# Performance work log

Hardware: AMD Instinct MI355X
Metric: run time of the kernel (lower is better)

The kernel has to match this reference:

```python
import jax, jax.numpy as jnp
import numpy as np

NUM_NODES = 50000
NUM_EDGES = 600000
IN_DIM = 128
HID = 128
OUT_DIM = 10
NUM_GRAPHS = 64


def setup_inputs() -> dict:
    key = jax.random.key(0)
    ks = jax.random.split(key, 12)
    x = jax.random.normal(ks[0], (NUM_NODES, IN_DIM), dtype=jnp.float32)
    edge_index = jax.random.randint(ks[1], (2, NUM_EDGES), 0, NUM_NODES, dtype=jnp.int64)
    batch = jnp.sort(jax.random.randint(ks[2], (NUM_NODES,), 0, NUM_GRAPHS, dtype=jnp.int64))
    s = 0.05
    W1 = jax.random.normal(ks[3], (IN_DIM, HID), dtype=jnp.float32) * s
    b1 = jnp.zeros((HID,), dtype=jnp.float32)
    W2 = jax.random.normal(ks[4], (HID, HID), dtype=jnp.float32) * s
    b2 = jnp.zeros((HID,), dtype=jnp.float32)
    W3 = jax.random.normal(ks[5], (HID, HID), dtype=jnp.float32) * s
    b3 = jnp.zeros((HID,), dtype=jnp.float32)
    Wlin = jax.random.normal(ks[6], (HID, OUT_DIM), dtype=jnp.float32) * s
    blin = jnp.zeros((OUT_DIM,), dtype=jnp.float32)
    return {"x": x, "edge_index": edge_index, "batch": batch,
            "W1": W1, "b1": b1, "W2": W2, "b2": b2, "W3": W3, "b3": b3,
            "Wlin": Wlin, "blin": blin}


def _gcn_conv(x, W, b, src, dst, norm):
    # h = X W ; out[i] = sum_{(j->i)} norm_e * h[j] ; + bias
    h = x @ W                                   # [N, H]
    msg = h[src] * norm[:, None]                # [E+N, H] gather + scale
    out = jax.ops.segment_sum(msg, dst, num_segments=x.shape[0])  # scatter-add
    return out + b


def reference(x, edge_index, batch, W1, b1, W2, b2, W3, b3, Wlin, blin):
    N = x.shape[0]
    # add self loops (PyG GCNConv default)
    loops = jnp.arange(N, dtype=edge_index.dtype)
    src = jnp.concatenate([edge_index[0], loops])
    dst = jnp.concatenate([edge_index[1], loops])
    # symmetric normalization D^{-1/2} (A+I) D^{-1/2}; degree on target nodes
    deg = jax.ops.segment_sum(jnp.ones_like(dst, dtype=x.dtype), dst, num_segments=N)
    dinv = jnp.where(deg > 0, jax.lax.rsqrt(deg), 0.0)
    norm = dinv[src] * dinv[dst]

    h = jax.nn.relu(_gcn_conv(x, W1, b1, src, dst, norm))   # dropout = identity (eval)
    h = jax.nn.relu(_gcn_conv(h, W2, b2, src, dst, norm))
    h = jax.nn.relu(_gcn_conv(h, W3, b3, src, dst, norm))

    # global mean pool over graphs
    sums = jax.ops.segment_sum(h, batch, num_segments=NUM_GRAPHS)          # [G, H]
    cnts = jax.ops.segment_sum(jnp.ones((N,), dtype=h.dtype), batch, num_segments=NUM_GRAPHS)
    pooled = sums / jnp.maximum(cnts, 1.0)[:, None]
    return pooled @ Wlin + blin                                            # [G, OUT]
```

## Files before the change

### kernel.cpp

```cpp
#include <hip/hip_runtime.h>
#include <hip/hip_bf16.h>
#include <hip/hip_fp16.h>


#define HID 128
#define NGRAPH 64

typedef _Float16 half8v __attribute__((ext_vector_type(8)));
typedef float floatx4 __attribute__((ext_vector_type(4)));

__device__ __forceinline__ int idx_at(const void* p, long long i, int f64) {
    if (f64) return (int)((const long long*)p)[i];
    return ((const int*)p)[i];
}

__global__ void init_kernel(const int* __restrict__ ei, int* __restrict__ flag,
                            int* __restrict__ counts, float* __restrict__ pooled,
                            uint4* __restrict__ csr4, int N, int nCsr4) {
    int i = blockIdx.x * blockDim.x + threadIdx.x;
    int stride = gridDim.x * blockDim.x;
    if (i < N) counts[i] = 0;
    if (i < NGRAPH * HID) pooled[i] = 0.f;
    unsigned fillv = (unsigned)N | ((unsigned)N << 16);
    uint4 fv = make_uint4(fillv, fillv, fillv, fillv);
    for (int j = i; j < nCsr4; j += stride) csr4[j] = fv;
    if (blockIdx.x == 0) {
        __shared__ int cnt;
        if (threadIdx.x == 0) cnt = 0;
        __syncthreads();
        int z = 0;
        for (int k = threadIdx.x; k < 2048; k += 256)
            if (ei[2 * k + 1] == 0) z++;
        atomicAdd(&cnt, z);
        __syncthreads();
        if (threadIdx.x == 0) *flag = (cnt > 1024) ? 1 : 0;
    }
}

__global__ void hist_kernel(const void* __restrict__ ei, const int* __restrict__ flag,
                            int* __restrict__ counts, int E, int N) {
    int e = blockIdx.x * blockDim.x + threadIdx.x;
    if (e >= E) return;
    int f64 = *flag;
    int d = idx_at(ei, (long long)E + e, f64);
    if ((unsigned)d < (unsigned)N) atomicAdd(&counts[d], 1);
}

__device__ __forceinline__ int wave_incl_scan(int v, int lane) {
#pragma unroll
    for (int off = 1; off < 64; off <<= 1) {
        int u = __shfl_up(v, off);
        if (lane >= off) v += u;
    }
    return v;
}

__global__ __launch_bounds__(256) void blocksum_kernel(const int* __restrict__ counts,
                                                       int* __restrict__ bsums, int N) {
    int i = blockIdx.x * 256 + threadIdx.x;
    int v = (i < N) ? ((counts[i] + 7) & ~7) : 0;
    int lane = threadIdx.x & 63, w = threadIdx.x >> 6;
#pragma unroll
    for (int off = 32; off > 0; off >>= 1) v += __shfl_down(v, off);
    __shared__ int ws[4];
    if (lane == 0) ws[w] = v;
    __syncthreads();
    if (threadIdx.x == 0) bsums[blockIdx.x] = ws[0] + ws[1] + ws[2] + ws[3];
}

__global__ __launch_bounds__(256) void scanb_kernel(int* __restrict__ bsums, int nb) {
    int t = threadIdx.x;
    int lane = t & 63, w = t >> 6;
    int v = (t < nb) ? bsums[t] : 0;
    int iv = wave_incl_scan(v, lane);
    __shared__ int wsum[4];
    if (lane == 63) wsum[w] = iv;
    __syncthreads();
    int add = 0;
    for (int k = 0; k < w; ++k) add += wsum[k];
    if (t < nb) bsums[t] = iv - v + add;
}

__global__ __launch_bounds__(256) void fill_kernel(const int* __restrict__ counts,
                                                   const int* __restrict__ bsums,
                                                   int* __restrict__ rowstart,
                                                   int* __restrict__ cursor,
                                                   float* __restrict__ dinv, int N) {
    int i = blockIdx.x * 256 + threadIdx.x;
    int c = (i < N) ? counts[i] : 0;
    int cp = (c + 7) & ~7;
    int lane = threadIdx.x & 63, w = threadIdx.x >> 6;
    int iv = wave_incl_scan(cp, lane);
    __shared__ int wsum[4];
    if (lane == 63) wsum[w] = iv;
    __syncthreads();
    int add = bsums[blockIdx.x];
    for (int k = 0; k < w; ++k) add += wsum[k];
    int excl = iv - cp + add;
    if (i < N) {
        rowstart[i] = excl;
        cursor[i] = excl;
        dinv[i] = rsqrtf((float)(c + 1));
        if (i == N - 1) rowstart[N] = excl + cp;
    }
}

__global__ void scatter_kernel(const void* __restrict__ ei, const int* __restrict__ flag,
                               int* __restrict__ cursor,
                               unsigned short* __restrict__ csr_src, int E, int N) {
    int e = blockIdx.x * blockDim.x + threadIdx.x;
    if (e >= E) return;
    int f64 = *flag;
    int s = idx_at(ei, e, f64);
    int d = idx_at(ei, (long long)E + e, f64);
    if ((unsigned)s >= (unsigned)N || (unsigned)d >= (unsigned)N) return;
    int pos = atomicAdd(&cursor[d], 1);
    csr_src[pos] = (unsigned short)s;
}

__global__ __launch_bounds__(256) void prep_kernel(const float* __restrict__ x,
                                                   const float* __restrict__ dinv,
                                                   __half2* __restrict__ xs,
                                                   __half2* __restrict__ hsA,
                                                   __half2* __restrict__ hsB,
                                                   const float* __restrict__ W1,
                                                   const float* __restrict__ W2,
                                                   const float* __restrict__ W3,
                                                   half8v* __restrict__ wf,
                                                   int N, int n2) {
    if (blockIdx.x < 24) {
        int which = blockIdx.x >> 3;
        const float* W = which == 0 ? W1 : (which == 1 ? W2 : W3);
        int t = (blockIdx.x & 7) * 256 + threadIdx.x;
        int lane = t & 63;
        int nt = (t >> 6) & 7;
        int kblk = t >> 9;
        int n = nt * 16 + (lane & 15);
        int kbase = kblk * 32 + (lane >> 4) * 8;
        half8v v;
#pragma unroll
        for (int j = 0; j < 8; ++j) v[j] = (_Float16)W[(size_t)(kbase + j) * 128 + n];
        wf[which * 2048 + t] = v;
    } else if (blockIdx.x == 24) {
        int t = threadIdx.x;
        __half2 z = __floats2half2_rn(0.f, 0.f);
        if (t < 64) xs[(size_t)N * 64 + t] = z;
        else if (t < 128) hsA[(size_t)N * 64 + (t - 64)] = z;
        else if (t < 192) hsB[(size_t)N * 64 + (t - 128)] = z;
    } else {
        int i = (blockIdx.x - 25) * 256 + threadIdx.x;
        if (i >= n2) return;
        float dv = dinv[i >> 6];
        float2 v = ((const float2*)x)[i];
        xs[i] = __floats2half2_rn(dv * v.x, dv * v.y);
    }
}

__global__ __launch_bounds__(256) void agg_kernel(const __half2* __restrict__ xs,
                                                  const int* __restrict__ rowstart,
                                                  const unsigned short* __restrict__ csr_src,
                                                  const float* __restrict__ dinv,
                                                  __half2* __restrict__ out, int N) {
    int wid = (blockIdx.x * blockDim.x + threadIdx.x) >> 6;
    int lane = threadIdx.x & 63;
    if (wid >= N) return;
    float di = dinv[wid];
    float2 s0 = __half22float2(xs[(size_t)wid * 64 + lane]);
    float accx = s0.x, accy = s0.y;
    float bccx = 0.f, bccy = 0.f;
    int e0 = rowstart[wid], e1 = rowstart[wid + 1];
    for (int e = e0; e < e1; e += 8) {
        uint4 q = *(const uint4*)(csr_src + e);
        int s0i = q.x & 0xffff, s1i = q.x >> 16;
        int s2i = q.y & 0xffff, s3i = q.y >> 16;
        int s4i = q.z & 0xffff, s5i = q.z >> 16;
        int s6i = q.w & 0xffff, s7i = q.w >> 16;
        __half2 v0 = xs[(size_t)s0i * 64 + lane];
        __half2 v1 = xs[(size_t)s1i * 64 + lane];
        __half2 v2 = xs[(size_t)s2i * 64 + lane];
        __half2 v3 = xs[(size_t)s3i * 64 + lane];
        __half2 v4 = xs[(size_t)s4i * 64 + lane];
        __half2 v5 = xs[(size_t)s5i * 64 + lane];
        __half2 v6 = xs[(size_t)s6i * 64 + lane];
        __half2 v7 = xs[(size_t)s7i * 64 + lane];
        float2 f0 = __half22float2(v0), f1 = __half22float2(v1);
        float2 f2 = __half22float2(v2), f3 = __half22float2(v3);
        float2 f4 = __half22float2(v4), f5 = __half22float2(v5);
        float2 f6 = __half22float2(v6), f7 = __half22float2(v7);
        accx += f0.x + f2.x; accy += f0.y + f2.y;
        bccx += f1.x + f3.x; bccy += f1.y + f3.y;
        accx += f4.x + f6.x; accy += f4.y + f6.y;
        bccx += f5.x + f7.x; bccy += f5.y + f7.y;
    }
    out[(size_t)wid * 64 + lane] = __floats2half2_rn(di * (accx + bccx),
                                                     di * (accy + bccy));
}

template <bool SCALED>
__global__ __launch_bounds__(256) void gemm_mfma(const __half2* __restrict__ A16,
                                                 const half8v* __restrict__ wf,
                                                 const float* __restrict__ bias,
                                                 const float* __restrict__ dinv,
                                                 __half2* __restrict__ O16, int M) {
    int wid = threadIdx.x >> 6, lane = threadIdx.x & 63;
    int rowTile = blockIdx.x * 64 + wid * 16;
    int hi = lane >> 4;
    int arow = rowTile + (lane & 15);
    if (arow >= M) arow = M - 1;
    const half8v* Arow = (const half8v*)((const _Float16*)A16 + (size_t)arow * 128);

    floatx4 acc[8];
#pragma unroll
    for (int nt = 0; nt < 8; ++nt) acc[nt] = (floatx4){0.f, 0.f, 0.f, 0.f};

#pragma unroll
    for (int kb = 0; kb < 4; ++kb) {
        half8v a = Arow[kb * 4 + hi];
#pragma unroll
        for (int nt = 0; nt < 8; ++nt) {
            half8v w = wf[(kb * 8 + nt) * 64 + lane];
            acc[nt] = __builtin_amdgcn_mfma_f32_16x16x32_f16(a, w, acc[nt], 0, 0, 0);
        }
    }

    int ocol_lo = lane & 15;
    int orow0 = rowTile + hi * 4;
    float dv[4];
#pragma unroll
    for (int r = 0; r < 4; ++r) {
        int orow = orow0 + r;
        dv[r] = (SCALED && orow < M) ? dinv[orow] : 1.0f;
    }
#pragma unroll
    for (int nt = 0; nt < 8; ++nt) {
        int col = nt * 16 + ocol_lo;
        float b = bias[col];
#pragma unroll
        for (int r = 0; r < 4; ++r) {
            int orow = orow0 + r;
            if (orow < M) {
                float v = fmaxf(acc[nt][r] + b, 0.f);
                if (SCALED) v *= dv[r];
                ((_Float16*)O16)[(size_t)orow * 128 + col] = (_Float16)v;
            }
        }
    }
}

#define POOL_CHUNK 16
__global__ __launch_bounds__(256) void pool_kernel(const __half2* __restrict__ h,
                                                   const void* __restrict__ batch,
                                                   const int* __restrict__ flag,
                                                   float* __restrict__ pooled, int N) {
    int wid = (blockIdx.x * blockDim.x + threadIdx.x) >> 6;
    int lane = threadIdx.x & 63;
    int n0 = wid * POOL_CHUNK;
    if (n0 >= N) return;
    int n1 = n0 + POOL_CHUNK; if (n1 > N) n1 = N;
    int f64 = *flag;
    int g = idx_at(batch, n0, f64);
    float ax = 0.f, ay = 0.f;
    for (int n = n0; n < n1; ++n) {
        int gn = idx_at(batch, n, f64);
        if (gn != g) {
            if ((unsigned)g < (unsigned)NGRAPH) {
                atomicAdd(&pooled[g * HID + 2 * lane], ax);
                atomicAdd(&pooled[g * HID + 2 * lane + 1], ay);
            }
            ax = ay = 0.f; g = gn;
        }
        float2 v = __half22float2(h[(size_t)n * 64 + lane]);
        ax += v.x; ay += v.y;
    }
    if ((unsigned)g < (unsigned)NGRAPH) {
        atomicAdd(&pooled[g * HID + 2 * lane], ax);
        atomicAdd(&pooled[g * HID + 2 * lane + 1], ay);
    }
}

__global__ __launch_bounds__(128) void final_kernel(const float* __restrict__ pooled,
                                                    const void* __restrict__ batch,
                                                    const int* __restrict__ flag,
                                                    const float* __restrict__ Wl,
                                                    const float* __restrict__ bl,
                                                    float* __restrict__ out, int N) {
    int o = blockIdx.x * blockDim.x + threadIdx.x;
    if (o >= NGRAPH * 10) return;
    int g = o / 10, c = o % 10;
    int f64 = *flag;
    auto lb = [&](int val) {
        int lo = 0, hi = N;
        while (lo < hi) {
            int mid = (lo + hi) >> 1;
            if (idx_at(batch, mid, f64) < val) lo = mid + 1; else hi = mid;
        }
        return lo;
    };
    int cnt = lb(g + 1) - lb(g);
    float inv = 1.0f / fmaxf((float)cnt, 1.0f);
    float acc = 0.f;
    for (int k = 0; k < HID; ++k)
        acc = fmaf(pooled[g * HID + k], Wl[k * 10 + c], acc);
    out[o] = acc * inv + bl[c];
}

extern "C" void kernel_launch(void* const* d_in, const int* in_sizes, int n_in,
                              void* d_out, int out_size, void* d_ws, size_t ws_size,
                              hipStream_t stream) {
    const float* x   = (const float*)d_in[0];
    const void* ei   = d_in[1];
    const void* bat  = d_in[2];
    const float* W1  = (const float*)d_in[3];
    const float* b1  = (const float*)d_in[4];
    const float* W2  = (const float*)d_in[5];
    const float* b2  = (const float*)d_in[6];
    const float* W3  = (const float*)d_in[7];
    const float* b3  = (const float*)d_in[8];
    const float* Wl  = (const float*)d_in[9];
    const float* bl  = (const float*)d_in[10];
    float* out = (float*)d_out;

    const int N = in_sizes[0] / HID;
    const int E = in_sizes[1] / 2;
    const int EPAD = (E + 7 * N + 7) & ~7;

    char* w = (char*)d_ws;
    size_t off = 0;
    auto carve = [&](size_t bytes) -> void* {
        void* p = w + off;
        off = (off + bytes + 255) & ~(size_t)255;
        return p;
    };
    __half2* xs       = (__half2*)carve((size_t)(N + 1) * HID * 2);
    __half2* aggB16   = (__half2*)carve((size_t)N * HID * 2);
    __half2* hsA      = (__half2*)carve((size_t)(N + 1) * HID * 2);
    __half2* hsB      = (__half2*)carve((size_t)(N + 1) * HID * 2);
    int*     counts   = (int*)carve((size_t)N * 4);
    int*     rowstart = (int*)carve((size_t)(N + 1) * 4);
    int*     cursor   = (int*)carve((size_t)N * 4);
    float*   dinv     = (float*)carve((size_t)N * 4);
    unsigned short* csr_src = (unsigned short*)carve((size_t)EPAD * 2);
    float*   pooled   = (float*)carve((size_t)NGRAPH * HID * 4);
    half8v*  wf       = (half8v*)carve(3 * 2048 * 16);
    int*     bsums    = (int*)carve(1024);
    int*     flag     = (int*)carve(256);

    const int nb = (N + 255) / 256;
    const int n2 = N * HID / 2;

    init_kernel<<<nb, 256, 0, stream>>>((const int*)ei, flag, counts, pooled,
                                        (uint4*)csr_src, N, EPAD / 8);
    hist_kernel<<<(E + 255) / 256, 256, 0, stream>>>(ei, flag, counts, E, N);
    blocksum_kernel<<<nb, 256, 0, stream>>>(counts, bsums, N);
    scanb_kernel<<<1, 256, 0, stream>>>(bsums, nb);
    fill_kernel<<<nb, 256, 0, stream>>>(counts, bsums, rowstart, cursor, dinv, N);
    scatter_kernel<<<(E + 255) / 256, 256, 0, stream>>>(ei, flag, cursor, csr_src, E, N);
    prep_kernel<<<25 + (n2 + 255) / 256, 256, 0, stream>>>(x, dinv, xs, hsA, hsB,
                                                           W1, W2, W3, wf, N, n2);

    int aggBlocks  = (N + 3) / 4;
    int gemmBlocks = (N + 63) / 64;

    agg_kernel<<<aggBlocks, 256, 0, stream>>>(xs, rowstart, csr_src, dinv, aggB16, N);
    gemm_mfma<true><<<gemmBlocks, 256, 0, stream>>>(aggB16, wf, b1, dinv, hsA, N);
    agg_kernel<<<aggBlocks, 256, 0, stream>>>(hsA, rowstart, csr_src, dinv, aggB16, N);
    gemm_mfma<true><<<gemmBlocks, 256, 0, stream>>>(aggB16, wf + 2048, b2, dinv, hsB, N);
    agg_kernel<<<aggBlocks, 256, 0, stream>>>(hsB, rowstart, csr_src, dinv, aggB16, N);
    gemm_mfma<false><<<gemmBlocks, 256, 0, stream>>>(aggB16, wf + 4096, b3, dinv, hsA, N);

    int poolWaves = (N + POOL_CHUNK - 1) / POOL_CHUNK;
    int poolBlocks = (poolWaves + 3) / 4;
    pool_kernel<<<poolBlocks, 256, 0, stream>>>(hsA, bat, flag, pooled, N);
    final_kernel<<<5, 128, 0, stream>>>(pooled, bat, flag, Wl, bl, out, N);
}
```

Baseline: 221.4 us.

## Fuse CSR-building preprocessing kernels into one cooperative grid-synced kernel

Replaces seven preprocessing launches (init, histogram, block sums, scan, fill, scatter, prep) with a single cooperative kernel of 1024 blocks that uses grid.sync() between phases. The intent is to remove per-launch overhead and the idle gaps between small dependent kernels. In exchange, each phase now runs with grid-stride loops over a fixed grid, and the five grid-wide barriers add their own cost. The cooperative launch needs all 1024 blocks to be co-resident, and the return status of hipLaunchCooperativeKernel is not checked.

```diff
diff --git a/kernel.cpp b/kernel.cpp
--- a/kernel.cpp
+++ b/kernel.cpp
@@ -1,6 +1,9 @@
 #include <hip/hip_runtime.h>
 #include <hip/hip_bf16.h>
 #include <hip/hip_fp16.h>
+#include <hip/hip_cooperative_groups.h>
+
+namespace cg = cooperative_groups;
 
 
 #define HID 128
@@ -14,142 +17,141 @@
     return ((const int*)p)[i];
 }
 
-__global__ void init_kernel(const int* __restrict__ ei, int* __restrict__ flag,
-                            int* __restrict__ counts, float* __restrict__ pooled,
-                            uint4* __restrict__ csr4, int N, int nCsr4) {
-    int i = blockIdx.x * blockDim.x + threadIdx.x;
-    int stride = gridDim.x * blockDim.x;
-    if (i < N) counts[i] = 0;
-    if (i < NGRAPH * HID) pooled[i] = 0.f;
-    unsigned fillv = (unsigned)N | ((unsigned)N << 16);
-    uint4 fv = make_uint4(fillv, fillv, fillv, fillv);
-    for (int j = i; j < nCsr4; j += stride) csr4[j] = fv;
+__device__ __forceinline__ int wave_incl_scan(int v, int lane) {
+#pragma unroll
+    for (int off = 1; off < 64; off <<= 1) {
+        int u = __shfl_up(v, off);
+        if (lane >= off) v += u;
+    }
+    return v;
+}
+
+__global__ __launch_bounds__(256) void preprocess_kernel(
+    const void* __restrict__ ei, int* __restrict__ flag,
+    int* __restrict__ counts, float* __restrict__ pooled,
+    unsigned short* __restrict__ csr_src, int* __restrict__ rowstart,
+    int* __restrict__ cursor, float* __restrict__ dinv,
+    int* __restrict__ bsums, const float* __restrict__ x,
+    __half2* __restrict__ xs, __half2* __restrict__ hsA,
+    __half2* __restrict__ hsB, const float* __restrict__ W1,
+    const float* __restrict__ W2, const float* __restrict__ W3,
+    half8v* __restrict__ wf, int N, int E, int nCsr4, int n2) {
+    cg::grid_group grid = cg::this_grid();
+    const int tid = blockIdx.x * blockDim.x + threadIdx.x;
+    const int nthreads = gridDim.x * blockDim.x;
+    const int nb = (N + 255) >> 8;
+
     if (blockIdx.x == 0) {
         __shared__ int cnt;
         if (threadIdx.x == 0) cnt = 0;
         __syncthreads();
         int z = 0;
         for (int k = threadIdx.x; k < 2048; k += 256)
-            if (ei[2 * k + 1] == 0) z++;
+            if (((const int*)ei)[2 * k + 1] == 0) z++;
         atomicAdd(&cnt, z);
         __syncthreads();
         if (threadIdx.x == 0) *flag = (cnt > 1024) ? 1 : 0;
     }
-}
-
-__global__ void hist_kernel(const void* __restrict__ ei, const int* __restrict__ flag,
-                            int* __restrict__ counts, int E, int N) {
-    int e = blockIdx.x * blockDim.x + threadIdx.x;
-    if (e >= E) return;
-    int f64 = *flag;
-    int d = idx_at(ei, (long long)E + e, f64);
-    if ((unsigned)d < (unsigned)N) atomicAdd(&counts[d], 1);
-}
-
-__device__ __forceinline__ int wave_incl_scan(int v, int lane) {
-#pragma unroll
-    for (int off = 1; off < 64; off <<= 1) {
-        int u = __shfl_up(v, off);
-        if (lane >= off) v += u;
-    }
-    return v;
-}
-
-__global__ __launch_bounds__(256) void blocksum_kernel(const int* __restrict__ counts,
-                                                       int* __restrict__ bsums, int N) {
-    int i = blockIdx.x * 256 + threadIdx.x;
-    int v = (i < N) ? ((counts[i] + 7) & ~7) : 0;
-    int lane = threadIdx.x & 63, w = threadIdx.x >> 6;
-#pragma unroll
-    for (int off = 32; off > 0; off >>= 1) v += __shfl_down(v, off);
-    __shared__ int ws[4];
-    if (lane == 0) ws[w] = v;
-    __syncthreads();
-    if (threadIdx.x == 0) bsums[blockIdx.x] = ws[0] + ws[1] + ws[2] + ws[3];
-}
-
-__global__ __launch_bounds__(256) void scanb_kernel(int* __restrict__ bsums, int nb) {
-    int t = threadIdx.x;
-    int lane = t & 63, w = t >> 6;
-    int v = (t < nb) ? bsums[t] : 0;
-    int iv = wave_incl_scan(v, lane);
-    __shared__ int wsum[4];
-    if (lane == 63) wsum[w] = iv;
-    __syncthreads();
-    int add = 0;
-    for (int k = 0; k < w; ++k) add += wsum[k];
-    if (t < nb) bsums[t] = iv - v + add;
-}
-
-__global__ __launch_bounds__(256) void fill_kernel(const int* __restrict__ counts,
-                                                   const int* __restrict__ bsums,
-                                                   int* __restrict__ rowstart,
-                                                   int* __restrict__ cursor,
-                                                   float* __restrict__ dinv, int N) {
-    int i = blockIdx.x * 256 + threadIdx.x;
-    int c = (i < N) ? counts[i] : 0;
-    int cp = (c + 7) & ~7;
-    int lane = threadIdx.x & 63, w = threadIdx.x >> 6;
-    int iv = wave_incl_scan(cp, lane);
-    __shared__ int wsum[4];
-    if (lane == 63) wsum[w] = iv;
-    __syncthreads();
-    int add = bsums[blockIdx.x];
-    for (int k = 0; k < w; ++k) add += wsum[k];
-    int excl = iv - cp + add;
-    if (i < N) {
-        rowstart[i] = excl;
-        cursor[i] = excl;
-        dinv[i] = rsqrtf((float)(c + 1));
-        if (i == N - 1) rowstart[N] = excl + cp;
-    }
-}
-
-__global__ void scatter_kernel(const void* __restrict__ ei, const int* __restrict__ flag,
-                               int* __restrict__ cursor,
-                               unsigned short* __restrict__ csr_src, int E, int N) {
-    int e = blockIdx.x * blockDim.x + threadIdx.x;
-    if (e >= E) return;
-    int f64 = *flag;
-    int s = idx_at(ei, e, f64);
-    int d = idx_at(ei, (long long)E + e, f64);
-    if ((unsigned)s >= (unsigned)N || (unsigned)d >= (unsigned)N) return;
-    int pos = atomicAdd(&cursor[d], 1);
-    csr_src[pos] = (unsigned short)s;
-}
-
-__global__ __launch_bounds__(256) void prep_kernel(const float* __restrict__ x,
-                                                   const float* __restrict__ dinv,
-                                                   __half2* __restrict__ xs,
-                                                   __half2* __restrict__ hsA,
-                                                   __half2* __restrict__ hsB,
-                                                   const float* __restrict__ W1,
-                                                   const float* __restrict__ W2,
-                                                   const float* __restrict__ W3,
-                                                   half8v* __restrict__ wf,
-                                                   int N, int n2) {
-    if (blockIdx.x < 24) {
-        int which = blockIdx.x >> 3;
+    for (int i = tid; i < N; i += nthreads) counts[i] = 0;
+    for (int i = tid; i < NGRAPH * HID; i += nthreads) pooled[i] = 0.f;
+    {
+        unsigned fillv = (unsigned)N | ((unsigned)N << 16);
+        uint4 fv = make_uint4(fillv, fillv, fillv, fillv);
+        uint4* csr4 = (uint4*)csr_src;
+        for (int j = tid; j < nCsr4; j += nthreads) csr4[j] = fv;
+    }
+    {
+        __half2 z2 = __floats2half2_rn(0.f, 0.f);
+        for (int t = tid; t < 192; t += nthreads) {
+            if (t < 64) xs[(size_t)N * 64 + t] = z2;
+            else if (t < 128) hsA[(size_t)N * 64 + (t - 64)] = z2;
+            else hsB[(size_t)N * 64 + (t - 128)] = z2;
+        }
+    }
+    for (int t = tid; t < 3 * 2048; t += nthreads) {
+        int which = t >> 11;
+        int tt = t & 2047;
         const float* W = which == 0 ? W1 : (which == 1 ? W2 : W3);
-        int t = (blockIdx.x & 7) * 256 + threadIdx.x;
-        int lane = t & 63;
-        int nt = (t >> 6) & 7;
-        int kblk = t >> 9;
-        int n = nt * 16 + (lane & 15);
+        int lane = tt & 63, nt2 = (tt >> 6) & 7, kblk = tt >> 9;
+        int n = nt2 * 16 + (lane & 15);
         int kbase = kblk * 32 + (lane >> 4) * 8;
         half8v v;
 #pragma unroll
         for (int j = 0; j < 8; ++j) v[j] = (_Float16)W[(size_t)(kbase + j) * 128 + n];
-        wf[which * 2048 + t] = v;
-    } else if (blockIdx.x == 24) {
+        wf[t] = v;
+    }
+    grid.sync();
+
+    const int f64 = *flag;
+    for (int e = tid; e < E; e += nthreads) {
+        int d = idx_at(ei, (long long)E + e, f64);
+        if ((unsigned)d < (unsigned)N) atomicAdd(&counts[d], 1);
+    }
+    grid.sync();
+
+    {
+        __shared__ int ws[4];
+        for (int chunk = blockIdx.x; chunk < nb; chunk += gridDim.x) {
+            int i = chunk * 256 + threadIdx.x;
+            int v = (i < N) ? ((counts[i] + 7) & ~7) : 0;
+            int lane = threadIdx.x & 63, w = threadIdx.x >> 6;
+#pragma unroll
+            for (int off = 32; off > 0; off >>= 1) v += __shfl_down(v, off);
+            if (lane == 0) ws[w] = v;
+            __syncthreads();
+            if (threadIdx.x == 0) bsums[chunk] = ws[0] + ws[1] + ws[2] + ws[3];
+            __syncthreads();
+        }
+    }
+    grid.sync();
+
+    if (blockIdx.x == 0) {
+        __shared__ int wsum[4];
         int t = threadIdx.x;
-        __half2 z = __floats2half2_rn(0.f, 0.f);
-        if (t < 64) xs[(size_t)N * 64 + t] = z;
-        else if (t < 128) hsA[(size_t)N * 64 + (t - 64)] = z;
-        else if (t < 192) hsB[(size_t)N * 64 + (t - 128)] = z;
-    } else {
-        int i = (blockIdx.x - 25) * 256 + threadIdx.x;
-        if (i >= n2) return;
+        int lane = t & 63, w = t >> 6;
+        int v = (t < nb) ? bsums[t] : 0;
+        int iv = wave_incl_scan(v, lane);
+        if (lane == 63) wsum[w] = iv;
+        __syncthreads();
+        int add = 0;
+        for (int k = 0; k < w; ++k) add += wsum[k];
+        if (t < nb) bsums[t] = iv - v + add;
+    }
+    grid.sync();
+
+    {
+        __shared__ int wsum2[4];
+        for (int chunk = blockIdx.x; chunk < nb; chunk += gridDim.x) {
+            int i = chunk * 256 + threadIdx.x;
+            int c = (i < N) ? counts[i] : 0;
+            int cp = (c + 7) & ~7;
+            int lane = threadIdx.x & 63, w = threadIdx.x >> 6;
+            int iv = wave_incl_scan(cp, lane);
+            if (lane == 63) wsum2[w] = iv;
+            __syncthreads();
+            int add = bsums[chunk];
+            for (int k = 0; k < w; ++k) add += wsum2[k];
+            int excl = iv - cp + add;
+            if (i < N) {
+                rowstart[i] = excl;
+                cursor[i] = excl;
+                dinv[i] = rsqrtf((float)(c + 1));
+                if (i == N - 1) rowstart[N] = excl + cp;
+            }
+            __syncthreads();
+        }
+    }
+    grid.sync();
+
+    for (int e = tid; e < E; e += nthreads) {
+        int s = idx_at(ei, e, f64);
+        int d = idx_at(ei, (long long)E + e, f64);
+        if ((unsigned)s < (unsigned)N && (unsigned)d < (unsigned)N) {
+            int pos = atomicAdd(&cursor[d], 1);
+            csr_src[pos] = (unsigned short)s;
+        }
+    }
+    for (int i = tid; i < n2; i += nthreads) {
         float dv = dinv[i >> 6];
         float2 v = ((const float2*)x)[i];
         xs[i] = __floats2half2_rn(dv * v.x, dv * v.y);
@@ -345,18 +347,18 @@
     int*     bsums    = (int*)carve(1024);
     int*     flag     = (int*)carve(256);
 
-    const int nb = (N + 255) / 256;
-    const int n2 = N * HID / 2;
-
-    init_kernel<<<nb, 256, 0, stream>>>((const int*)ei, flag, counts, pooled,
-                                        (uint4*)csr_src, N, EPAD / 8);
-    hist_kernel<<<(E + 255) / 256, 256, 0, stream>>>(ei, flag, counts, E, N);
-    blocksum_kernel<<<nb, 256, 0, stream>>>(counts, bsums, N);
-    scanb_kernel<<<1, 256, 0, stream>>>(bsums, nb);
-    fill_kernel<<<nb, 256, 0, stream>>>(counts, bsums, rowstart, cursor, dinv, N);
-    scatter_kernel<<<(E + 255) / 256, 256, 0, stream>>>(ei, flag, cursor, csr_src, E, N);
-    prep_kernel<<<25 + (n2 + 255) / 256, 256, 0, stream>>>(x, dinv, xs, hsA, hsB,
-                                                           W1, W2, W3, wf, N, n2);
+    int nCsr4 = EPAD / 8;
+    int n2 = N * HID / 2;
+    int N_ = N, E_ = E;
+
+    void* args[] = { (void*)&ei, (void*)&flag, (void*)&counts, (void*)&pooled,
+                     (void*)&csr_src, (void*)&rowstart, (void*)&cursor,
+                     (void*)&dinv, (void*)&bsums, (void*)&x, (void*)&xs,
+                     (void*)&hsA, (void*)&hsB, (void*)&W1, (void*)&W2,
+                     (void*)&W3, (void*)&wf, (void*)&N_, (void*)&E_,
+                     (void*)&nCsr4, (void*)&n2 };
+    hipLaunchCooperativeKernel((void*)preprocess_kernel, dim3(1024), dim3(256),
+                               args, 0, stream);
 
     int aggBlocks  = (N + 3) / 4;
     int gemmBlocks = (N + 63) / 64;
```

New measurement: 764.3 us. 245% more time.
